# Kernel tuning notes

Hardware: AMD Instinct MI355X
Metric: run time of the kernel (lower is better)

## Reference

```python
import jax, jax.numpy as jnp
import numpy as np


def setup_inputs() -> dict:
    key = jax.random.key(0)
    ks = jax.random.split(key, 6)
    B, C, S, E = 8, 16, 512, 256
    wscale = (2.0 / (E + E)) ** 0.5  # xavier_normal for [E, E] fan_in=fan_out=E
    return {
        "query": jax.random.normal(ks[0], (B, C, S, E), dtype=jnp.float32),
        "key": jax.random.normal(ks[1], (B, C, S, E), dtype=jnp.float32),
        "value": jax.random.normal(ks[2], (B, C, S, E), dtype=jnp.float32),
        "q_proj_weight": jax.random.normal(ks[3], (C, E, E), dtype=jnp.float32) * wscale,
        "k_proj_weight": jax.random.normal(ks[4], (C, E, E), dtype=jnp.float32) * wscale,
        "v_proj_weight": jax.random.normal(ks[5], (C, E, E), dtype=jnp.float32) * wscale,
        "q_proj_bias": jnp.zeros((C, 1, E), dtype=jnp.float32),
        "k_proj_bias": jnp.zeros((C, 1, E), dtype=jnp.float32),
        "v_proj_bias": jnp.zeros((C, 1, E), dtype=jnp.float32),
    }


def reference(query, key, value, q_proj_weight, k_proj_weight, v_proj_weight,
              q_proj_bias, k_proj_bias, v_proj_bias):
    E = query.shape[-1]
    # Per-cycle projection + bias + ReLU.  b=batch, c=cycle, s/t=seq, e/f=embed
    q = jax.nn.relu(jnp.einsum("bcse,cef->bcsf", query, q_proj_weight) + q_proj_bias)
    k = jax.nn.relu(jnp.einsum("bcse,cef->bcsf", key, k_proj_weight) + k_proj_bias)
    v = jax.nn.relu(jnp.einsum("bcse,cef->bcsf", value, v_proj_weight) + v_proj_bias)
    q = q * (float(E) ** -0.5)
    attn = jax.nn.softmax(jnp.einsum("bcse,bcte->bcst", q, k), axis=-1)
    out = jnp.einsum("bcst,bcte->bcse", attn, v)
    return out
```

## Files before the change

kernel.cpp:

```cpp
#include <hip/hip_runtime.h>

constexpr int BATCH = 8;
constexpr int CYC   = 16;
constexpr int SEQ   = 512;
constexpr int EMB   = 256;

typedef __attribute__((ext_vector_type(8))) short bf16x8;
typedef __attribute__((ext_vector_type(4))) float f32x4;

__device__ __forceinline__ unsigned short f2bf(float x) {
    unsigned int u = __float_as_uint(x);
    u += 0x7fffu + ((u >> 16) & 1u);
    return (unsigned short)(u >> 16);
}

__device__ __forceinline__ f32x4 mfma16(bf16x8 a, bf16x8 b, f32x4 c) {
    return __builtin_amdgcn_mfma_f32_16x16x32_bf16(a, b, c, 0, 0, 0);
}

__device__ __forceinline__ void gll16(const unsigned short* g, unsigned short* l) {
    __builtin_amdgcn_global_load_lds(
        (const __attribute__((address_space(1))) void*)g,
        (__attribute__((address_space(3))) void*)l, 16, 0, 0);
}

__global__ __launch_bounds__(256) void conv_kernel(const float* __restrict__ X,
                                                   unsigned short* __restrict__ Y) {
    const size_t i = ((size_t)blockIdx.x * 256 + threadIdx.x) * 8;
    const float4 a = *(const float4*)(X + i);
    const float4 b = *(const float4*)(X + i + 4);
    ushort4 o0, o1;
    o0.x = f2bf(a.x); o0.y = f2bf(a.y); o0.z = f2bf(a.z); o0.w = f2bf(a.w);
    o1.x = f2bf(b.x); o1.y = f2bf(b.y); o1.z = f2bf(b.z); o1.w = f2bf(b.w);
    *(ushort4*)(Y + i)     = o0;
    *(ushort4*)(Y + i + 4) = o1;
}

__global__ __launch_bounds__(256) void wt_kernel(const float* __restrict__ W,
                                                 unsigned short* __restrict__ Wt) {
    __shared__ float tile[64][65];
    const int c  = blockIdx.z;
    const int e0 = blockIdx.x * 64;
    const int f0 = blockIdx.y * 64;
    const float* Wc = W + (size_t)c * EMB * EMB;
    unsigned short* Wtc = Wt + (size_t)c * EMB * EMB;
    const int t = threadIdx.x;
    {
        const int er = t >> 4;
        const int fc = (t & 15) * 4;
        for (int i = 0; i < 4; ++i) {
            const float4 v = *(const float4*)(Wc + (size_t)(e0 + er + i * 16) * EMB + f0 + fc);
            tile[er + i * 16][fc + 0] = v.x;
            tile[er + i * 16][fc + 1] = v.y;
            tile[er + i * 16][fc + 2] = v.z;
            tile[er + i * 16][fc + 3] = v.w;
        }
    }
    __syncthreads();
    {
        const int fr = t >> 4;
        const int ec = (t & 15) * 4;
        for (int i = 0; i < 4; ++i) {
            const int f = fr + i * 16;
            ushort4 o;
            o.x = f2bf(tile[ec + 0][f]);
            o.y = f2bf(tile[ec + 1][f]);
            o.z = f2bf(tile[ec + 2][f]);
            o.w = f2bf(tile[ec + 3][f]);
            *(ushort4*)(Wtc + (size_t)(f0 + f) * EMB + e0 + ec) = o;
        }
    }
}

__global__ __launch_bounds__(256) void proj_kernel(
    const unsigned short* __restrict__ Xbf, const unsigned short* __restrict__ Wt,
    const float* __restrict__ bias, unsigned short* __restrict__ Y,
    const float scale, const int transposeOut)
{
    __shared__ unsigned short smem[8192];
    unsigned short* As = smem;
    unsigned short* Bs = smem + 4096;
    const int bc = blockIdx.x;
    const int c  = bc & (CYC - 1);
    const int n0 = blockIdx.y * 128;
    const int m0 = blockIdx.z * 128;
    const unsigned short* Xb = Xbf + (size_t)bc * SEQ * EMB;
    const unsigned short* Wc = Wt + (size_t)c * EMB * EMB;
    const float* bb = bias + (size_t)c * EMB;
    unsigned short* Yb = Y + (size_t)bc * SEQ * EMB;

    const int tid  = threadIdx.x;
    const int lane = tid & 63, w = tid >> 6;
    const int ln   = lane & 15, quad = lane >> 4;
    const int wm   = w >> 1, wn = w & 1;
    const int wu   = __builtin_amdgcn_readfirstlane(w);

    f32x4 acc[4][4];
    for (int i = 0; i < 4; ++i)
        for (int j = 0; j < 4; ++j) acc[i][j] = (f32x4){0.f, 0.f, 0.f, 0.f};

    for (int kk = 0; kk < 8; ++kk) {
        const int k0 = kk * 32;
        const unsigned short* ga = Xb + (size_t)(m0 + lane) * EMB + k0 + wu * 8;
        gll16(ga,            As + (wu * 128) * 8);
        gll16(ga + 64 * EMB, As + (wu * 128 + 64) * 8);
        const unsigned short* gb = Wc + (size_t)(n0 + lane) * EMB + k0 + wu * 8;
        gll16(gb,            Bs + (wu * 128) * 8);
        gll16(gb + 64 * EMB, Bs + (wu * 128 + 64) * 8);
        __syncthreads();
        bf16x8 af[4], bfv[4];
        for (int i = 0; i < 4; ++i)
            af[i] = *(const bf16x8*)&As[(quad * 128 + wm * 64 + i * 16 + ln) * 8];
        for (int j = 0; j < 4; ++j)
            bfv[j] = *(const bf16x8*)&Bs[(quad * 128 + wn * 64 + j * 16 + ln) * 8];
        for (int i = 0; i < 4; ++i)
            for (int j = 0; j < 4; ++j)
                acc[i][j] = mfma16(af[i], bfv[j], acc[i][j]);
        __syncthreads();
    }

    float bvj[4];
    for (int j = 0; j < 4; ++j) bvj[j] = bb[n0 + wn * 64 + j * 16 + ln];

    if (!transposeOut) {
        unsigned short* ep = smem + w * 1152;
        for (int i = 0; i < 4; ++i) {
            for (int j = 0; j < 4; ++j)
                for (int r = 0; r < 4; ++r)
                    ep[(quad * 4 + r) * 72 + j * 16 + ln] =
                        f2bf(fmaxf(acc[i][j][r] + bvj[j], 0.f) * scale);
            __syncthreads();
            for (int h = 0; h < 2; ++h) {
                const int cid = lane + h * 64;
                const int row = cid >> 3, ch = cid & 7;
                *(bf16x8*)&Yb[(size_t)(m0 + wm * 64 + i * 16 + row) * EMB +
                              n0 + wn * 64 + ch * 8] = *(const bf16x8*)&ep[row * 72 + ch * 8];
            }
            __syncthreads();
        }
    } else {
        for (int j = 0; j < 4; ++j) {
            const int fg = n0 + wn * 64 + j * 16 + ln;
            for (int i = 0; i < 4; ++i) {
                const int mb = m0 + wm * 64 + i * 16 + quad * 4;
                ushort4 u;
                u.x = f2bf(fmaxf(acc[i][j][0] + bvj[j], 0.f) * scale);
                u.y = f2bf(fmaxf(acc[i][j][1] + bvj[j], 0.f) * scale);
                u.z = f2bf(fmaxf(acc[i][j][2] + bvj[j], 0.f) * scale);
                u.w = f2bf(fmaxf(acc[i][j][3] + bvj[j], 0.f) * scale);
                *(ushort4*)&Yb[(size_t)fg * SEQ + mb] = u;
            }
        }
    }
}

__global__ __launch_bounds__(256) void attn_kernel(
    const unsigned short* __restrict__ Qp, const unsigned short* __restrict__ Kp,
    const unsigned short* __restrict__ Vt, float* __restrict__ Out)
{
    __shared__ unsigned short Ks[32][264];
    __shared__ unsigned short Vs[256][40];
    __shared__ unsigned short Ps[64][40];
    const int bc = blockIdx.x;
    const int qt = blockIdx.y;
    const unsigned short* Qb = Qp + (size_t)bc * SEQ * EMB;
    const unsigned short* Kb = Kp + (size_t)bc * SEQ * EMB;
    const unsigned short* Vb = Vt + (size_t)bc * SEQ * EMB;
    float* Ob = Out + (size_t)bc * SEQ * EMB;

    const int tid  = threadIdx.x;
    const int lane = tid & 63, w = tid >> 6;
    const int ln   = lane & 15, quad = lane >> 4;

    bf16x8 qf[8];
    const int qrow = qt * 64 + w * 16 + ln;
    for (int ke = 0; ke < 8; ++ke)
        qf[ke] = *(const bf16x8*)(Qb + (size_t)qrow * EMB + ke * 32 + quad * 8);

    f32x4 of[16];
    for (int n = 0; n < 16; ++n) of[n] = (f32x4){0.f, 0.f, 0.f, 0.f};
    float lsum[4] = {0.f, 0.f, 0.f, 0.f};

    for (int tt = 0; tt < 16; ++tt) {
        const int t0 = tt * 32;
        for (int i = 0; i < 4; ++i) {
            const int idx = tid + i * 256;
            const int r = idx >> 5, c8 = (idx & 31) * 8;
            *(bf16x8*)&Ks[r][c8] = *(const bf16x8*)(Kb + (size_t)(t0 + r) * EMB + c8);
        }
        for (int i = 0; i < 4; ++i) {
            const int idx = tid + i * 256;
            const int e = idx >> 2, c8 = (idx & 3) * 8;
            *(bf16x8*)&Vs[e][c8] = *(const bf16x8*)(Vb + (size_t)e * SEQ + t0 + c8);
        }
        __syncthreads();

        f32x4 sf0 = (f32x4){0.f,0.f,0.f,0.f}, sf1 = (f32x4){0.f,0.f,0.f,0.f};
        for (int ke = 0; ke < 8; ++ke) {
            bf16x8 b0 = *(const bf16x8*)&Ks[ln][ke * 32 + quad * 8];
            bf16x8 b1 = *(const bf16x8*)&Ks[16 + ln][ke * 32 + quad * 8];
            sf0 = mfma16(qf[ke], b0, sf0);
            sf1 = mfma16(qf[ke], b1, sf1);
        }

        float p0[4], p1[4];
        for (int r = 0; r < 4; ++r) {
            p0[r] = __expf(sf0[r]);
            p1[r] = __expf(sf1[r]);
            lsum[r] += p0[r] + p1[r];
        }
        for (int r = 0; r < 4; ++r) {
            Ps[w * 16 + quad * 4 + r][ln]      = f2bf(p0[r]);
            Ps[w * 16 + quad * 4 + r][16 + ln] = f2bf(p1[r]);
        }
        __syncthreads();

        bf16x8 af = *(const bf16x8*)&Ps[w * 16 + ln][quad * 8];
        for (int n = 0; n < 16; ++n) {
            bf16x8 bv = *(const bf16x8*)&Vs[n * 16 + ln][quad * 8];
            of[n] = mfma16(af, bv, of[n]);
        }
        __syncthreads();
    }

    for (int off = 1; off < 16; off <<= 1)
        for (int r = 0; r < 4; ++r)
            lsum[r] += __shfl_xor(lsum[r], off, 64);
    float inv[4];
    for (int r = 0; r < 4; ++r) inv[r] = 1.0f / lsum[r];
    const int mbase = qt * 64 + w * 16 + quad * 4;
    for (int n = 0; n < 16; ++n)
        for (int r = 0; r < 4; ++r)
            Ob[(size_t)(mbase + r) * EMB + n * 16 + ln] = of[n][r] * inv[r];
}

extern "C" void kernel_launch(void* const* d_in, const int* in_sizes, int n_in,
                              void* d_out, int out_size, void* d_ws, size_t ws_size,
                              hipStream_t stream) {
    const float* query = (const float*)d_in[0];
    const float* key_  = (const float*)d_in[1];
    const float* value = (const float*)d_in[2];
    const float* wq = (const float*)d_in[3];
    const float* wk = (const float*)d_in[4];
    const float* wv = (const float*)d_in[5];
    const float* bq = (const float*)d_in[6];
    const float* bk = (const float*)d_in[7];
    const float* bv = (const float*)d_in[8];
    float* out = (float*)d_out;

    char* ws = (char*)d_ws;
    const size_t wsz = (size_t)CYC * EMB * EMB * sizeof(unsigned short);
    const size_t psz = (size_t)BATCH * CYC * SEQ * EMB * sizeof(unsigned short);
    unsigned short* Wtq = (unsigned short*)(ws);
    unsigned short* Wtk = (unsigned short*)(ws + wsz);
    unsigned short* Wtv = (unsigned short*)(ws + 2 * wsz);
    unsigned short* Qp  = (unsigned short*)(ws + 3 * wsz);
    unsigned short* Kp  = (unsigned short*)(ws + 3 * wsz + psz);
    unsigned short* Vtp = (unsigned short*)(ws + 3 * wsz + 2 * psz);
    unsigned short* Xbf = (unsigned short*)(ws + 3 * wsz + 3 * psz);

    const dim3 tb(256);
    const int N = BATCH * CYC * SEQ * EMB;
    const int cgrid = N / (8 * 256);

    wt_kernel<<<dim3(4, 4, CYC), tb, 0, stream>>>(wq, Wtq);
    wt_kernel<<<dim3(4, 4, CYC), tb, 0, stream>>>(wk, Wtk);
    wt_kernel<<<dim3(4, 4, CYC), tb, 0, stream>>>(wv, Wtv);

    const dim3 pg(BATCH * CYC, 2, 4);
    conv_kernel<<<cgrid, tb, 0, stream>>>(query, Xbf);
    proj_kernel<<<pg, tb, 0, stream>>>(Xbf, Wtq, bq, Qp, 0.0625f, 0);
    conv_kernel<<<cgrid, tb, 0, stream>>>(key_, Xbf);
    proj_kernel<<<pg, tb, 0, stream>>>(Xbf, Wtk, bk, Kp, 1.0f, 0);
    conv_kernel<<<cgrid, tb, 0, stream>>>(value, Xbf);
    proj_kernel<<<pg, tb, 0, stream>>>(Xbf, Wtv, bv, Vtp, 1.0f, 1);

    attn_kernel<<<dim3(BATCH * CYC, SEQ / 64), tb, 0, stream>>>(Qp, Kp, Vtp, out);
}
```

Baseline: 383.0 us.

## Fuse fp32-to-bf16 input conversion into projection kernel with full-width N tiles

```diff
diff --git a/kernel.cpp b/kernel.cpp
--- a/kernel.cpp
+++ b/kernel.cpp
@@ -13,6 +13,9 @@
     u += 0x7fffu + ((u >> 16) & 1u);
     return (unsigned short)(u >> 16);
 }
+__device__ __forceinline__ unsigned int pk2(float lo, float hi) {
+    return (unsigned int)f2bf(lo) | ((unsigned int)f2bf(hi) << 16);
+}
 
 __device__ __forceinline__ f32x4 mfma16(bf16x8 a, bf16x8 b, f32x4 c) {
     return __builtin_amdgcn_mfma_f32_16x16x32_bf16(a, b, c, 0, 0, 0);
@@ -22,18 +25,6 @@
     __builtin_amdgcn_global_load_lds(
         (const __attribute__((address_space(1))) void*)g,
         (__attribute__((address_space(3))) void*)l, 16, 0, 0);
-}
-
-__global__ __launch_bounds__(256) void conv_kernel(const float* __restrict__ X,
-                                                   unsigned short* __restrict__ Y) {
-    const size_t i = ((size_t)blockIdx.x * 256 + threadIdx.x) * 8;
-    const float4 a = *(const float4*)(X + i);
-    const float4 b = *(const float4*)(X + i + 4);
-    ushort4 o0, o1;
-    o0.x = f2bf(a.x); o0.y = f2bf(a.y); o0.z = f2bf(a.z); o0.w = f2bf(a.w);
-    o1.x = f2bf(b.x); o1.y = f2bf(b.y); o1.z = f2bf(b.z); o1.w = f2bf(b.w);
-    *(ushort4*)(Y + i)     = o0;
-    *(ushort4*)(Y + i + 4) = o1;
 }
 
 __global__ __launch_bounds__(256) void wt_kernel(const float* __restrict__ W,
@@ -73,18 +64,17 @@
 }
 
 __global__ __launch_bounds__(256) void proj_kernel(
-    const unsigned short* __restrict__ Xbf, const unsigned short* __restrict__ Wt,
+    const float* __restrict__ X, const unsigned short* __restrict__ Wt,
     const float* __restrict__ bias, unsigned short* __restrict__ Y,
     const float scale, const int transposeOut)
 {
-    __shared__ unsigned short smem[8192];
+    __shared__ unsigned short smem[10752];
     unsigned short* As = smem;
-    unsigned short* Bs = smem + 4096;
+    unsigned short* Bs = smem + 2560;
     const int bc = blockIdx.x;
     const int c  = bc & (CYC - 1);
-    const int n0 = blockIdx.y * 128;
-    const int m0 = blockIdx.z * 128;
-    const unsigned short* Xb = Xbf + (size_t)bc * SEQ * EMB;
+    const int m0 = blockIdx.y * 64;
+    const float* Xb = X + (size_t)bc * SEQ * EMB;
     const unsigned short* Wc = Wt + (size_t)c * EMB * EMB;
     const float* bb = bias + (size_t)c * EMB;
     unsigned short* Yb = Y + (size_t)bc * SEQ * EMB;
@@ -92,8 +82,13 @@
     const int tid  = threadIdx.x;
     const int lane = tid & 63, w = tid >> 6;
     const int ln   = lane & 15, quad = lane >> 4;
-    const int wm   = w >> 1, wn = w & 1;
     const int wu   = __builtin_amdgcn_readfirstlane(w);
+
+    const int arow = tid >> 2;
+    const int acol = (tid & 3) * 8;
+    const int brow = lane >> 2;
+    const int gch  = (lane & 3) ^ ((lane >> 3) & 3);
+    const int bslot = quad ^ ((ln >> 1) & 3);
 
     f32x4 acc[4][4];
     for (int i = 0; i < 4; ++i)
@@ -101,18 +96,24 @@
 
     for (int kk = 0; kk < 8; ++kk) {
         const int k0 = kk * 32;
-        const unsigned short* ga = Xb + (size_t)(m0 + lane) * EMB + k0 + wu * 8;
-        gll16(ga,            As + (wu * 128) * 8);
-        gll16(ga + 64 * EMB, As + (wu * 128 + 64) * 8);
-        const unsigned short* gb = Wc + (size_t)(n0 + lane) * EMB + k0 + wu * 8;
-        gll16(gb,            Bs + (wu * 128) * 8);
-        gll16(gb + 64 * EMB, Bs + (wu * 128 + 64) * 8);
+        const float* ax = Xb + (size_t)(m0 + arow) * EMB + k0 + acol;
+        const float4 a0 = *(const float4*)ax;
+        const float4 a1 = *(const float4*)(ax + 4);
+        int4 pk;
+        pk.x = pk2(a0.x, a0.y); pk.y = pk2(a0.z, a0.w);
+        pk.z = pk2(a1.x, a1.y); pk.w = pk2(a1.z, a1.w);
+        *(int4*)&As[arow * 40 + acol] = pk;
+        for (int j = 0; j < 4; ++j) {
+            const int r = wu * 64 + j * 16 + brow;
+            gll16(Wc + (size_t)r * EMB + k0 + gch * 8,
+                  Bs + (size_t)(wu * 64 + j * 16) * 32);
+        }
         __syncthreads();
         bf16x8 af[4], bfv[4];
         for (int i = 0; i < 4; ++i)
-            af[i] = *(const bf16x8*)&As[(quad * 128 + wm * 64 + i * 16 + ln) * 8];
+            af[i] = *(const bf16x8*)&As[(i * 16 + ln) * 40 + quad * 8];
         for (int j = 0; j < 4; ++j)
-            bfv[j] = *(const bf16x8*)&Bs[(quad * 128 + wn * 64 + j * 16 + ln) * 8];
+            bfv[j] = *(const bf16x8*)&Bs[(w * 64 + j * 16 + ln) * 32 + bslot * 8];
         for (int i = 0; i < 4; ++i)
             for (int j = 0; j < 4; ++j)
                 acc[i][j] = mfma16(af[i], bfv[j], acc[i][j]);
@@ -120,7 +121,7 @@
     }
 
     float bvj[4];
-    for (int j = 0; j < 4; ++j) bvj[j] = bb[n0 + wn * 64 + j * 16 + ln];
+    for (int j = 0; j < 4; ++j) bvj[j] = bb[w * 64 + j * 16 + ln];
 
     if (!transposeOut) {
         unsigned short* ep = smem + w * 1152;
@@ -133,16 +134,16 @@
             for (int h = 0; h < 2; ++h) {
                 const int cid = lane + h * 64;
                 const int row = cid >> 3, ch = cid & 7;
-                *(bf16x8*)&Yb[(size_t)(m0 + wm * 64 + i * 16 + row) * EMB +
-                              n0 + wn * 64 + ch * 8] = *(const bf16x8*)&ep[row * 72 + ch * 8];
+                *(bf16x8*)&Yb[(size_t)(m0 + i * 16 + row) * EMB + w * 64 + ch * 8] =
+                    *(const bf16x8*)&ep[row * 72 + ch * 8];
             }
             __syncthreads();
         }
     } else {
         for (int j = 0; j < 4; ++j) {
-            const int fg = n0 + wn * 64 + j * 16 + ln;
+            const int fg = w * 64 + j * 16 + ln;
             for (int i = 0; i < 4; ++i) {
-                const int mb = m0 + wm * 64 + i * 16 + quad * 4;
+                const int mb = m0 + i * 16 + quad * 4;
                 ushort4 u;
                 u.x = f2bf(fmaxf(acc[i][j][0] + bvj[j], 0.f) * scale);
                 u.y = f2bf(fmaxf(acc[i][j][1] + bvj[j], 0.f) * scale);
@@ -257,23 +258,16 @@
     unsigned short* Qp  = (unsigned short*)(ws + 3 * wsz);
     unsigned short* Kp  = (unsigned short*)(ws + 3 * wsz + psz);
     unsigned short* Vtp = (unsigned short*)(ws + 3 * wsz + 2 * psz);
-    unsigned short* Xbf = (unsigned short*)(ws + 3 * wsz + 3 * psz);
 
     const dim3 tb(256);
-    const int N = BATCH * CYC * SEQ * EMB;
-    const int cgrid = N / (8 * 256);
-
     wt_kernel<<<dim3(4, 4, CYC), tb, 0, stream>>>(wq, Wtq);
     wt_kernel<<<dim3(4, 4, CYC), tb, 0, stream>>>(wk, Wtk);
     wt_kernel<<<dim3(4, 4, CYC), tb, 0, stream>>>(wv, Wtv);
 
-    const dim3 pg(BATCH * CYC, 2, 4);
-    conv_kernel<<<cgrid, tb, 0, stream>>>(query, Xbf);
-    proj_kernel<<<pg, tb, 0, stream>>>(Xbf, Wtq, bq, Qp, 0.0625f, 0);
-    conv_kernel<<<cgrid, tb, 0, stream>>>(key_, Xbf);
-    proj_kernel<<<pg, tb, 0, stream>>>(Xbf, Wtk, bk, Kp, 1.0f, 0);
-    conv_kernel<<<cgrid, tb, 0, stream>>>(value, Xbf);
-    proj_kernel<<<pg, tb, 0, stream>>>(Xbf, Wtv, bv, Vtp, 1.0f, 1);
+    const dim3 pg(BATCH * CYC, SEQ / 64);
+    proj_kernel<<<pg, tb, 0, stream>>>(query, Wtq, bq, Qp, 0.0625f, 0);
+    proj_kernel<<<pg, tb, 0, stream>>>(key_,  Wtk, bk, Kp, 1.0f, 0);
+    proj_kernel<<<pg, tb, 0, stream>>>(value, Wtv, bv, Vtp, 1.0f, 1);
 
     attn_kernel<<<dim3(BATCH * CYC, SEQ / 64), tb, 0, stream>>>(Qp, Kp, Vtp, out);
 }
```

New measurement: 352.4 us. -8.0%, faster.
